# Kernel tuning notes

Measured on AMD Instinct MI355X. Metric: run time of the kernel, lower is better.

Reference implementation:

```python
import jax, jax.numpy as jnp
import numpy as np

N, E1, E2, P, H = 4096, 131072, 131072, 65536, 128
ROLE_VOCAB, ROLE_DIM, IDX_VOCAB, IDX_DIM = 8, 16, 1024, 8


def _lin_init(key, fan_in, fan_out):
    k1, k2 = jax.random.split(key)
    bound = 1.0 / np.sqrt(fan_in)
    W = jax.random.uniform(k1, (fan_in, fan_out), jnp.float32, -bound, bound)
    b = jax.random.uniform(k2, (fan_out,), jnp.float32, -bound, bound)
    return W, b


def setup_inputs() -> dict:
    key = jax.random.key(0)
    ks = jax.random.split(key, 24)
    d = {}
    d["block_features"] = jax.random.normal(ks[0], (N, 16), jnp.float32)
    d["role_ids"] = jax.random.randint(ks[1], (N,), 0, ROLE_VOCAB)
    d["b2b_src"] = jax.random.randint(ks[2], (E1,), 0, N)
    d["b2b_dst"] = jax.random.randint(ks[3], (E1,), 0, N)
    d["b2b_w"] = jax.random.uniform(ks[4], (E1,), jnp.float32)
    d["p2b_pin"] = jax.random.randint(ks[5], (E2,), 0, P)
    d["p2b_block"] = jax.random.randint(ks[6], (E2,), 0, N)
    d["p2b_w"] = jax.random.uniform(ks[7], (E2,), jnp.float32)
    d["pins_pos"] = jax.random.normal(ks[8], (P, 2), jnp.float32)
    d["area_targets"] = jax.random.uniform(ks[9], (N,), jnp.float32)
    # parameters
    d["role_emb"] = jax.random.normal(ks[10], (ROLE_VOCAB, ROLE_DIM), jnp.float32)
    d["idx_emb"] = jax.random.normal(ks[11], (IDX_VOCAB, IDX_DIM), jnp.float32)
    d["in_W1"], d["in_b1"] = _lin_init(ks[12], 16 + IDX_DIM + ROLE_DIM, H)
    d["in_W2"], d["in_b2"] = _lin_init(ks[13], H, H)
    d["b2b_W1"], d["b2b_b1"] = _lin_init(ks[14], 2 * H + 1, H)
    d["b2b_W2"], d["b2b_b2"] = _lin_init(ks[15], H, H)
    d["p2b_W1"], d["p2b_b1"] = _lin_init(ks[16], H + 3, H)
    d["p2b_W2"], d["p2b_b2"] = _lin_init(ks[17], H, H)
    d["self_W"], d["self_b"] = _lin_init(ks[18], H, H)
    d["ln_g"] = jnp.ones((H,), jnp.float32)
    d["ln_b"] = jnp.zeros((H,), jnp.float32)
    d["gp_W1"], d["gp_b1"] = _lin_init(ks[19], 2 * H, H)
    d["gp_W2"], d["gp_b2"] = _lin_init(ks[20], H, H)
    return d


def _mlp2(x, W1, b1, W2, b2):
    return jax.nn.relu(x @ W1 + b1) @ W2 + b2


def _forward(block_features, role_ids, b2b_src, b2b_dst, b2b_w, p2b_pin, p2b_block,
             p2b_w, pins_pos, area_targets, role_emb, idx_emb, in_W1, in_b1, in_W2,
             in_b2, b2b_W1, b2b_b1, b2b_W2, b2b_b2, p2b_W1, p2b_b1, p2b_W2, p2b_b2,
             self_W, self_b, ln_g, ln_b, gp_W1, gp_b1, gp_W2, gp_b2):
    n = block_features.shape[0]
    role_e = role_emb[role_ids]                       # [N, role_dim]
    idx_e = idx_emb[jnp.arange(n) % IDX_VOCAB]        # [N, idx_dim]
    x = jnp.concatenate([block_features, role_e, idx_e], axis=-1)
    h = jax.nn.relu(_mlp2(x, in_W1, in_b1, in_W2, in_b2))  # input_proj ends in ReLU

    # --- b2b messages: two directed messages per undirected edge ---
    max_b2b = jax.lax.stop_gradient(jnp.maximum(jnp.max(jnp.abs(b2b_w)), 1.0))
    w = (b2b_w / max_b2b)[:, None]                    # [E1, 1]
    hi, hj = h[b2b_src], h[b2b_dst]                   # [E1, H]
    m_ij = _mlp2(jnp.concatenate([hi, hj, w], -1), b2b_W1, b2b_b1, b2b_W2, b2b_b2)
    m_ji = _mlp2(jnp.concatenate([hj, hi, w], -1), b2b_W1, b2b_b1, b2b_W2, b2b_b2)
    agg = jnp.zeros_like(h).at[b2b_src].add(m_ij).at[b2b_dst].add(m_ji)

    # --- p2b messages ---
    total_area = jnp.maximum(jnp.sum(area_targets), 1e-6)
    case_scale = jax.lax.stop_gradient(jnp.maximum(jnp.sqrt(total_area), 1e-6))
    max_p2b = jax.lax.stop_gradient(jnp.maximum(jnp.max(jnp.abs(p2b_w)), 1.0))
    pin_feats = jnp.concatenate(
        [pins_pos[p2b_pin] / case_scale, (p2b_w / max_p2b)[:, None]], axis=-1)  # [E2, 3]
    m_p = _mlp2(jnp.concatenate([h[p2b_block], pin_feats], -1),
                p2b_W1, p2b_b1, p2b_W2, p2b_b2)
    agg = agg.at[p2b_block].add(m_p)

    # --- combine + LayerNorm ---
    z = h @ self_W + self_b + agg
    mu = jnp.mean(z, axis=-1, keepdims=True)
    var = jnp.mean(jnp.square(z - mu), axis=-1, keepdims=True)
    block_embeddings = (z - mu) / jnp.sqrt(var + 1e-5) * ln_g + ln_b

    pooled = jnp.concatenate(
        [block_embeddings.mean(axis=0), block_embeddings.max(axis=0)], axis=-1)
    graph_embedding = _mlp2(pooled, gp_W1, gp_b1, gp_W2, gp_b2)
    return block_embeddings, graph_embedding


def reference(block_features, role_ids, b2b_src, b2b_dst, b2b_w, p2b_pin, p2b_block,
              p2b_w, pins_pos, area_targets, role_emb, idx_emb, in_W1, in_b1, in_W2,
              in_b2, b2b_W1, b2b_b1, b2b_W2, b2b_b2, p2b_W1, p2b_b1, p2b_W2, p2b_b2,
              self_W, self_b, ln_g, ln_b, gp_W1, gp_b1, gp_W2, gp_b2):
    block_embeddings, graph_embedding = _forward(
        block_features, role_ids, b2b_src, b2b_dst, b2b_w, p2b_pin, p2b_block,
        p2b_w, pins_pos, area_targets, role_emb, idx_emb, in_W1, in_b1, in_W2,
        in_b2, b2b_W1, b2b_b1, b2b_W2, b2b_b2, p2b_W1, p2b_b1, p2b_W2, p2b_b2,
        self_W, self_b, ln_g, ln_b, gp_W1, gp_b1, gp_W2, gp_b2)
    block_mask = jnp.ones((block_features.shape[0],), dtype=bool)
    return block_embeddings, graph_embedding, block_mask
```

## Files before the change

kernel.cpp:

```cpp
#include <hip/hip_runtime.h>
#include <hip/hip_bf16.h>

#define N_NODES 4096
#define HDIM    128
#define E1      131072
#define E2      131072
#define NMSG_B2B (2 * E1)
#define CAPB    192
#define CAPP    96
#define STGB    128
#define STGP    64

#define OFF_CNTB   8
#define OFF_CNTP   (OFF_CNTB + 4096)
#define OFF_RED    (OFF_CNTP + 4096)
#define OFF_PSUM   (OFF_RED + 96)
#define OFF_PMAX   (OFF_PSUM + 128)
#define OFF_HB     (OFF_PMAX + 128)
#define OFF_P      (OFF_HB + 262144)
#define OFF_Q      (OFF_P + 524288)
#define OFF_R      (OFF_Q + 524288)
#define OFF_CP     (OFF_R + 524288)
#define OFF_B2H    (OFF_CP + 24576)
#define OFF_B2L    (OFF_B2H + 8192)
#define OFF_P2H    (OFF_B2L + 8192)
#define OFF_P2L    (OFF_P2H + 8192)
#define OFF_SWP    (OFF_P2L + 8192)
#define OFF_IW1    (OFF_SWP + 8192)
#define OFF_IW2    (OFF_IW1 + 4096)
#define OFF_WLAST  (OFF_IW2 + 8192)
#define OFF_PEXTRA (OFF_WLAST + 128)
#define OFF_BKB    (OFF_PEXTRA + 384)
#define OFF_BKP    (OFF_BKB + 2 * N_NODES * CAPB)
#define WS_FLOATS  (OFF_BKP + 2 * N_NODES * CAPP)

typedef short short8 __attribute__((ext_vector_type(8)));
typedef float f32x4 __attribute__((ext_vector_type(4)));

__device__ __forceinline__ unsigned short f2bf(float f) {
  union { float f; unsigned u; } v; v.f = f;
  unsigned r = v.u + 0x7fffu + ((v.u >> 16) & 1u);
  return (unsigned short)(r >> 16);
}
__device__ __forceinline__ float bf2f(unsigned short h) {
  return __uint_as_float((unsigned)h << 16);
}
__device__ __forceinline__ int il(int c) { return ((c & 63) << 1) | (c >> 6); }
__device__ __forceinline__ f32x4 relu4(f32x4 v) {
  f32x4 r;
  r[0] = fmaxf(v[0], 0.f); r[1] = fmaxf(v[1], 0.f);
  r[2] = fmaxf(v[2], 0.f); r[3] = fmaxf(v[3], 0.f);
  return r;
}

__global__ __launch_bounds__(256) void setup_kernel(const float* __restrict__ b2bw,
                                                    const float* __restrict__ p2bw,
                                                    const float* __restrict__ area,
                                                    const float* __restrict__ bW1,
                                                    const float* __restrict__ bW2,
                                                    const float* __restrict__ pW1,
                                                    const float* __restrict__ pW2,
                                                    const float* __restrict__ sWm,
                                                    const float* __restrict__ iW1,
                                                    const float* __restrict__ iW2,
                                                    const int* __restrict__ src,
                                                    const int* __restrict__ dst,
                                                    const int* __restrict__ pblk,
                                                    const int* __restrict__ ppin,
                                                    const float* __restrict__ pins,
                                                    float* __restrict__ ws) {
  __shared__ float red[256];
  int b = blockIdx.x, t = threadIdx.x;
  if (b < 32) {
    float m = 0.f;
    for (int i = b * 256 + t; i < E1; i += 32 * 256) m = fmaxf(m, fabsf(b2bw[i]));
    red[t] = m; __syncthreads();
    for (int s = 128; s > 0; s >>= 1) { if (t < s) red[t] = fmaxf(red[t], red[t + s]); __syncthreads(); }
    if (t == 0) ws[OFF_RED + b] = red[0];
  } else if (b < 64) {
    float m = 0.f;
    for (int i = (b - 32) * 256 + t; i < E2; i += 32 * 256) m = fmaxf(m, fabsf(p2bw[i]));
    red[t] = m; __syncthreads();
    for (int s = 128; s > 0; s >>= 1) { if (t < s) red[t] = fmaxf(red[t], red[t + s]); __syncthreads(); }
    if (t == 0) ws[OFF_RED + b] = red[0];
  } else if (b < 96) {
    float s0 = 0.f;
    for (int i = (b - 64) * 256 + t; i < N_NODES; i += 32 * 256) s0 += area[i];
    red[t] = s0; __syncthreads();
    for (int s = 128; s > 0; s >>= 1) { if (t < s) red[t] += red[t + s]; __syncthreads(); }
    if (t == 0) ws[OFF_RED + b] = red[0];
  } else if (b == 96) {
    if (t < HDIM) {
      ws[OFF_PSUM + t] = 0.f;
      ((int*)ws)[OFF_PMAX + t] = 0x80000000;
    }
  } else if (b < 225) {
    unsigned short* Cp  = (unsigned short*)(ws + OFF_CP);
    unsigned short* B2h = (unsigned short*)(ws + OFF_B2H);
    unsigned short* B2l = (unsigned short*)(ws + OFF_B2L);
    unsigned short* P2h = (unsigned short*)(ws + OFF_P2H);
    unsigned short* P2l = (unsigned short*)(ws + OFF_P2L);
    unsigned short* Swp = (unsigned short*)(ws + OFF_SWP);
    unsigned short* I1p = (unsigned short*)(ws + OFF_IW1);
    unsigned short* I2p = (unsigned short*)(ws + OFF_IW2);
    float* wlast = ws + OFF_WLAST;
    float* pextra = ws + OFF_PEXTRA;
    const int total = 156160;
    for (int x = (b - 97) * 256 + t; x < total; x += 128 * 256) {
      if (x < 49152) {
        int j = x & 7, lane = (x >> 3) & 63, ks = (x >> 9) & 3, nc = x >> 11;
        int col = nc * 16 + (lane & 15), k = ks * 32 + (lane >> 4) * 8 + j;
        float v;
        if (col < 128)      v = bW1[k * 128 + col];
        else if (col < 256) v = bW1[(128 + k) * 128 + (col - 128)];
        else                v = pW1[k * 128 + (col - 256)];
        Cp[x] = f2bf(v);
      } else if (x < 114688) {
        int u = (x - 49152) & 16383, which = (x - 49152) >> 14;
        int j = u & 7, lane = (u >> 3) & 63, ks = (u >> 9) & 3, nt = u >> 11;
        int n = nt * 16 + (lane & 15), k = ks * 32 + (lane >> 4) * 8 + j;
        float v = (which < 2) ? bW2[k * 128 + n] : pW2[k * 128 + n];
        unsigned short hi = f2bf(v);
        unsigned short outv = (which & 1) ? f2bf(v - bf2f(hi)) : hi;
        ((which < 2) ? ((which & 1) ? B2l : B2h) : ((which & 1) ? P2l : P2h))[u] = outv;
      } else if (x < 131072) {
        int u = x - 114688;
        int j = u & 7, lane = (u >> 3) & 63, ks = (u >> 9) & 3, nt = u >> 11;
        int n = nt * 16 + (lane & 15), k = ks * 32 + (lane >> 4) * 8 + j;
        Swp[u] = f2bf(sWm[k * 128 + n]);
      } else if (x < 139264) {
        int u = x - 131072;
        int j = u & 7, lane = (u >> 3) & 63, ks = (u >> 9) & 1, nt = u >> 10;
        int n = nt * 16 + (lane & 15), k = ks * 32 + (lane >> 4) * 8 + j;
        I1p[u] = (k < 40) ? f2bf(iW1[k * 128 + n]) : 0;
      } else if (x < 155648) {
        int u = x - 139264;
        int j = u & 7, lane = (u >> 3) & 63, ks = (u >> 9) & 3, nt = u >> 11;
        int n = nt * 16 + (lane & 15), k = ks * 32 + (lane >> 4) * 8 + j;
        I2p[u] = f2bf(iW2[k * 128 + n]);
      } else if (x < 155776) {
        int c = x - 155648;
        wlast[il(c)] = bW1[256 * 128 + c];
      } else {
        int u = x - 155776;
        int r = u >> 7, c = u & 127;
        pextra[r * 128 + il(c)] = pW1[(128 + r) * 128 + c];
      }
    }
  } else {
    int i = (b - 225) * 256 + t;
    int* cntB = (int*)ws + OFF_CNTB;
    int* cntP = (int*)ws + OFF_CNTP;
    uint2* BKB = (uint2*)((int*)ws + OFF_BKB);
    uint2* BKP = (uint2*)((int*)ws + OFF_BKP);
    if (i < NMSG_B2B) {
      int e = i >> 1, d = i & 1;
      int tg = d ? dst[e] : src[e];
      int o  = d ? src[e] : dst[e];
      int pos = atomicAdd(&cntB[tg], 1);
      if (pos < CAPB) {
        uint2 v; v.x = (unsigned)o; v.y = __float_as_uint(b2bw[e]);
        BKB[tg * CAPB + pos] = v;
      }
    } else {
      int e = i - NMSG_B2B;
      int pin = ppin[e];
      int tg = pblk[e];
      int pos = atomicAdd(&cntP[tg], 1);
      if (pos < CAPP) {
        uint2 v;
        v.x = ((unsigned)f2bf(pins[pin * 2 + 1]) << 16) | (unsigned)f2bf(pins[pin * 2]);
        v.y = __float_as_uint(p2bw[e]);
        BKP[tg * CAPP + pos] = v;
      }
    }
  }
}

__global__ __launch_bounds__(512) void mid_kernel(const float* __restrict__ bfeat,
                                                  const int* __restrict__ rid,
                                                  const float* __restrict__ remb,
                                                  const float* __restrict__ iemb,
                                                  const float* __restrict__ ib1,
                                                  const float* __restrict__ ib2,
                                                  const float* __restrict__ bb1,
                                                  const float* __restrict__ pb1,
                                                  float* __restrict__ ws,
                                                  unsigned short* __restrict__ hb) {
  __shared__ __attribute__((aligned(16))) unsigned short xs[16 * 72];
  __shared__ __attribute__((aligned(16))) unsigned short h1s[16 * 136];
  __shared__ __attribute__((aligned(16))) unsigned short hs[16 * 136];
  int tid = threadIdx.x;
  const unsigned short* I1p = (const unsigned short*)(ws + OFF_IW1);
  const unsigned short* I2p = (const unsigned short*)(ws + OFF_IW2);
  const unsigned short* Cp  = (const unsigned short*)(ws + OFF_CP);
  float* P = ws + OFF_P;
  float* Q = ws + OFF_Q;
  float* R = ws + OFF_R;
  int n0 = blockIdx.x * 16;
  for (int idx = tid; idx < 1024; idx += 512) {
    int m = idx >> 6, c = idx & 63;
    int n = n0 + m;
    float v = 0.f;
    if (c < 16)      v = bfeat[n * 16 + c];
    else if (c < 32) v = remb[rid[n] * 16 + (c - 16)];
    else if (c < 40) v = iemb[(n & 1023) * 8 + (c - 32)];
    xs[m * 72 + c] = f2bf(v);
  }
  __syncthreads();
  int lane = tid & 63, wv = tid >> 6;
  int l15 = lane & 15, q = lane >> 4;
  f32x4 zero = {0.f, 0.f, 0.f, 0.f};
  f32x4 a1 = zero;
#pragma unroll
  for (int ks = 0; ks < 2; ks++) {
    short8 af = *(const short8*)(&xs[l15 * 72 + ks * 32 + q * 8]);
    short8 bfr = *(const short8*)(I1p + ((wv * 2 + ks) * 64 + lane) * 8);
    a1 = __builtin_amdgcn_mfma_f32_16x16x32_bf16(af, bfr, a1, 0, 0, 0);
  }
  {
    int n = wv * 16 + l15;
    float b = ib1[n];
#pragma unroll
    for (int r = 0; r < 4; r++)
      h1s[(q * 4 + r) * 136 + n] = f2bf(fmaxf(a1[r] + b, 0.f));
  }
  __syncthreads();
  f32x4 a2 = zero;
#pragma unroll
  for (int ks = 0; ks < 4; ks++) {
    short8 af = *(const short8*)(&h1s[l15 * 136 + ks * 32 + q * 8]);
    short8 bfr = *(const short8*)(I2p + ((wv * 4 + ks) * 64 + lane) * 8);
    a2 = __builtin_amdgcn_mfma_f32_16x16x32_bf16(af, bfr, a2, 0, 0, 0);
  }
  {
    int n = wv * 16 + l15;
    float b = ib2[n];
#pragma unroll
    for (int r = 0; r < 4; r++) {
      unsigned short hv = f2bf(fmaxf(a2[r] + b, 0.f));
      hs[(q * 4 + r) * 136 + n] = hv;
      hb[(n0 + q * 4 + r) * 128 + n] = hv;
    }
  }
  __syncthreads();
  f32x4 a3[3];
#pragma unroll
  for (int i = 0; i < 3; i++) a3[i] = zero;
#pragma unroll
  for (int ks = 0; ks < 4; ks++) {
    short8 af = *(const short8*)(&hs[l15 * 136 + ks * 32 + q * 8]);
#pragma unroll
    for (int j = 0; j < 3; j++) {
      short8 bfr = *(const short8*)(Cp + (((3 * wv + j) * 4 + ks) * 64 + lane) * 8);
      a3[j] = __builtin_amdgcn_mfma_f32_16x16x32_bf16(af, bfr, a3[j], 0, 0, 0);
    }
  }
#pragma unroll
  for (int j = 0; j < 3; j++) {
    int col = (3 * wv + j) * 16 + l15;
    int arr = col >> 7, cc = col & 127;
    float bias = (arr == 0) ? bb1[cc] : ((arr == 2) ? pb1[cc] : 0.f);
    float* dstp = (arr == 0) ? P : ((arr == 1) ? Q : R);
    int ic = il(cc);
#pragma unroll
    for (int r = 0; r < 4; r++)
      dstp[(n0 + q * 4 + r) * 128 + ic] = a3[j][r] + bias;
  }
}

__global__ __launch_bounds__(1024) void fused_kernel(const unsigned short* __restrict__ hb,
                                                     const float* __restrict__ sb,
                                                     const float* __restrict__ lng,
                                                     const float* __restrict__ lnb,
                                                     const float* __restrict__ bb2,
                                                     const float* __restrict__ pb2,
                                                     const float* __restrict__ gW1,
                                                     const float* __restrict__ gb1,
                                                     const float* __restrict__ gW2,
                                                     const float* __restrict__ gb2,
                                                     float* __restrict__ ws,
                                                     float* __restrict__ out) {
  __shared__ __attribute__((aligned(16))) unsigned short A[16 * 648];
  __shared__ __attribute__((aligned(16))) union {
    struct { float zp[2][16 * 128]; float zs[16 * 133]; } t;
    struct { uint2 bkb[16][STGB]; uint2 bkp[16][STGP]; } e;
  } U;
  __shared__ float muS[16], rsg[16];
  __shared__ float partS[16][16], partQ[16][16];
  __shared__ float psumL[8][128];
  __shared__ int   pmaxL[8][128];
  __shared__ float sInvB, sInvP, sInvC;
  __shared__ int   isLast;
  int tid = threadIdx.x;
  int n0 = blockIdx.x * 16;
  int lane = tid & 63, wv = tid >> 6;
  const int* cntBp = (const int*)ws + OFF_CNTB;
  const int* cntPp = (const int*)ws + OFF_CNTP;
  const uint2* BKB = (const uint2*)((const int*)ws + OFF_BKB);
  const uint2* BKP = (const uint2*)((const int*)ws + OFF_BKP);
  if (tid < 256) {
    int m = tid >> 4, o = (tid & 15) * 8;
    *(uint4*)(&A[m * 648 + o]) = *(const uint4*)(hb + (n0 + m) * 128 + o);
  }
  for (int idx = tid; idx < 16 * STGB; idx += 1024) {
    int m = idx >> 7, j = idx & (STGB - 1);
    if (j < cntBp[n0 + m]) U.e.bkb[m][j] = BKB[(n0 + m) * CAPB + j];
  }
  {
    int m = tid >> 6, j = tid & (STGP - 1);
    if (tid < 16 * STGP && j < cntPp[n0 + m]) U.e.bkp[m][j] = BKP[(n0 + m) * CAPP + j];
  }
  if (tid < 96) {
    float v = ws[OFF_RED + tid];
    if (tid < 64) {
#pragma unroll
      for (int s = 1; s < 32; s <<= 1) v = fmaxf(v, __shfl_xor(v, s, 64));
      if (tid == 0)  sInvB = 1.f / fmaxf(v, 1.f);
      if (tid == 32) sInvP = 1.f / fmaxf(v, 1.f);
    } else {
#pragma unroll
      for (int s = 1; s < 32; s <<= 1) v += __shfl_xor(v, s, 64);
      if (tid == 64) {
        float cs = fmaxf(sqrtf(fmaxf(v, 1e-6f)), 1e-6f);
        sInvC = 1.f / cs;
      }
    }
  }
  int l5 = lane & 31, hf = lane >> 5;
  f32x4 wl = *(const f32x4*)(ws + OFF_WLAST + 4 * l5);
  f32x4 e0 = *(const f32x4*)(ws + OFF_PEXTRA + 4 * l5);
  f32x4 e1 = *(const f32x4*)(ws + OFF_PEXTRA + 128 + 4 * l5);
  f32x4 e2 = *(const f32x4*)(ws + OFF_PEXTRA + 256 + 4 * l5);
  __syncthreads();
  {
    const float* Pm = ws + OFF_P;
    const float* Qm = ws + OFF_Q;
    const float* Rm = ws + OFF_R;
    float invb = sInvB, invp = sInvP, invc = sInvC;
    wl *= invb; e0 *= invc; e1 *= invc; e2 *= invp;
    int ln = wv;
    int node = n0 + ln;
    {
      int cnt = min(cntBp[node], CAPB);
      int stg = min(cnt, STGB);
      const uint2* bkL = U.e.bkb[ln];
      const uint2* bkG = BKB + node * CAPB;
      f32x4 p4 = *(const f32x4*)(Pm + node * 128 + 4 * l5);
      f32x4 acc = {0.f, 0.f, 0.f, 0.f};
      int m = 0;
      for (; m + 16 <= stg; m += 16) {
        uint2 k0 = bkL[m + hf],      k1 = bkL[m + 2 + hf];
        uint2 k2 = bkL[m + 4 + hf],  k3 = bkL[m + 6 + hf];
        uint2 k4 = bkL[m + 8 + hf],  k5 = bkL[m + 10 + hf];
        uint2 k6 = bkL[m + 12 + hf], k7 = bkL[m + 14 + hf];
        f32x4 q0 = *(const f32x4*)(Qm + k0.x * 128 + 4 * l5);
        f32x4 q1 = *(const f32x4*)(Qm + k1.x * 128 + 4 * l5);
        f32x4 q2 = *(const f32x4*)(Qm + k2.x * 128 + 4 * l5);
        f32x4 q3 = *(const f32x4*)(Qm + k3.x * 128 + 4 * l5);
        f32x4 q4 = *(const f32x4*)(Qm + k4.x * 128 + 4 * l5);
        f32x4 q5 = *(const f32x4*)(Qm + k5.x * 128 + 4 * l5);
        f32x4 q6 = *(const f32x4*)(Qm + k6.x * 128 + 4 * l5);
        f32x4 q7 = *(const f32x4*)(Qm + k7.x * 128 + 4 * l5);
        acc += relu4(p4 + __uint_as_float(k0.y) * wl + q0);
        acc += relu4(p4 + __uint_as_float(k1.y) * wl + q1);
        acc += relu4(p4 + __uint_as_float(k2.y) * wl + q2);
        acc += relu4(p4 + __uint_as_float(k3.y) * wl + q3);
        acc += relu4(p4 + __uint_as_float(k4.y) * wl + q4);
        acc += relu4(p4 + __uint_as_float(k5.y) * wl + q5);
        acc += relu4(p4 + __uint_as_float(k6.y) * wl + q6);
        acc += relu4(p4 + __uint_as_float(k7.y) * wl + q7);
      }
      for (; m + 8 <= stg; m += 8) {
        uint2 k0 = bkL[m + hf],     k1 = bkL[m + 2 + hf];
        uint2 k2 = bkL[m + 4 + hf], k3 = bkL[m + 6 + hf];
        f32x4 q0 = *(const f32x4*)(Qm + k0.x * 128 + 4 * l5);
        f32x4 q1 = *(const f32x4*)(Qm + k1.x * 128 + 4 * l5);
        f32x4 q2 = *(const f32x4*)(Qm + k2.x * 128 + 4 * l5);
        f32x4 q3 = *(const f32x4*)(Qm + k3.x * 128 + 4 * l5);
        acc += relu4(p4 + __uint_as_float(k0.y) * wl + q0);
        acc += relu4(p4 + __uint_as_float(k1.y) * wl + q1);
        acc += relu4(p4 + __uint_as_float(k2.y) * wl + q2);
        acc += relu4(p4 + __uint_as_float(k3.y) * wl + q3);
      }
      for (; m + 2 <= stg; m += 2) {
        uint2 k = bkL[m + hf];
        f32x4 q = *(const f32x4*)(Qm + k.x * 128 + 4 * l5);
        acc += relu4(p4 + __uint_as_float(k.y) * wl + q);
      }
      if (m < stg) {
        uint2 k = bkL[m + hf];
        f32x4 q = *(const f32x4*)(Qm + (k.x & (N_NODES - 1)) * 128 + 4 * l5);
        f32x4 v = relu4(p4 + __uint_as_float(k.y) * wl + q);
        if (hf == 0) acc += v;
        m++;
      }
      for (; m + 2 <= cnt; m += 2) {
        uint2 k = bkG[m + hf];
        f32x4 q = *(const f32x4*)(Qm + k.x * 128 + 4 * l5);
        acc += relu4(p4 + __uint_as_float(k.y) * wl + q);
      }
      if (m < cnt) {
        uint2 k = bkG[m + hf];
        f32x4 q = *(const f32x4*)(Qm + (k.x & (N_NODES - 1)) * 128 + 4 * l5);
        f32x4 v = relu4(p4 + __uint_as_float(k.y) * wl + q);
        if (hf == 0) acc += v;
      }
      f32x4 tot;
#pragma unroll
      for (int j = 0; j < 4; j++) tot[j] = acc[j] + __shfl_xor(acc[j], 32, 64);
      if (hf == 0) {
        unsigned short h0 = f2bf(tot[0]), h1 = f2bf(tot[1]);
        unsigned short h2 = f2bf(tot[2]), h3 = f2bf(tot[3]);
        *(unsigned*)(&A[ln * 648 + 128 + 2 * l5])      = (unsigned)h0 | ((unsigned)h2 << 16);
        *(unsigned*)(&A[ln * 648 + 128 + 64 + 2 * l5]) = (unsigned)h1 | ((unsigned)h3 << 16);
        unsigned short g0 = f2bf(tot[0] - bf2f(h0)), g1 = f2bf(tot[1] - bf2f(h1));
        unsigned short g2 = f2bf(tot[2] - bf2f(h2)), g3 = f2bf(tot[3] - bf2f(h3));
        *(unsigned*)(&A[ln * 648 + 256 + 2 * l5])      = (unsigned)g0 | ((unsigned)g2 << 16);
        *(unsigned*)(&A[ln * 648 + 256 + 64 + 2 * l5]) = (unsigned)g1 | ((unsigned)g3 << 16);
      }
    }
    {
      int cnt = min(cntPp[node], CAPP);
      int stg = min(cnt, STGP);
      const uint2* bkL = U.e.bkp[ln];
      const uint2* bkG = BKP + node * CAPP;
      f32x4 r4 = *(const f32x4*)(Rm + node * 128 + 4 * l5);
      f32x4 acc = {0.f, 0.f, 0.f, 0.f};
      int m = 0;
      for (; m + 4 <= stg; m += 4) {
        uint2 ka = bkL[m + hf], kb = bkL[m + 2 + hf];
        float a0 = __uint_as_float((ka.x & 0xFFFFu) << 16);
        float a1 = __uint_as_float(ka.x & 0xFFFF0000u);
        float a2 = __uint_as_float(ka.y);
        float b0 = __uint_as_float((kb.x & 0xFFFFu) << 16);
        float b1 = __uint_as_float(kb.x & 0xFFFF0000u);
        float b2 = __uint_as_float(kb.y);
        acc += relu4(r4 + a0 * e0 + a1 * e1 + a2 * e2);
        acc += relu4(r4 + b0 * e0 + b1 * e1 + b2 * e2);
      }
      for (; m + 2 <= stg; m += 2) {
        uint2 ka = bkL[m + hf];
        float a0 = __uint_as_float((ka.x & 0xFFFFu) << 16);
        float a1 = __uint_as_float(ka.x & 0xFFFF0000u);
        float a2 = __uint_as_float(ka.y);
        acc += relu4(r4 + a0 * e0 + a1 * e1 + a2 * e2);
      }
      if (m < stg) {
        uint2 ka = bkL[m + hf];
        float a0 = __uint_as_float((ka.x & 0xFFFFu) << 16);
        float a1 = __uint_as_float(ka.x & 0xFFFF0000u);
        float a2 = __uint_as_float(ka.y);
        f32x4 v = relu4(r4 + a0 * e0 + a1 * e1 + a2 * e2);
        if (hf == 0) acc += v;
        m++;
      }
      for (; m + 2 <= cnt; m += 2) {
        uint2 ka = bkG[m + hf];
        float a0 = __uint_as_float((ka.x & 0xFFFFu) << 16);
        float a1 = __uint_as_float(ka.x & 0xFFFF0000u);
        float a2 = __uint_as_float(ka.y);
        acc += relu4(r4 + a0 * e0 + a1 * e1 + a2 * e2);
      }
      if (m < cnt) {
        uint2 ka = bkG[m + hf];
        float a0 = __uint_as_float((ka.x & 0xFFFFu) << 16);
        float a1 = __uint_as_float(ka.x & 0xFFFF0000u);
        float a2 = __uint_as_float(ka.y);
        f32x4 v = relu4(r4 + a0 * e0 + a1 * e1 + a2 * e2);
        if (hf == 0) acc += v;
      }
      f32x4 tot;
#pragma unroll
      for (int j = 0; j < 4; j++) tot[j] = acc[j] + __shfl_xor(acc[j], 32, 64);
      if (hf == 0) {
        unsigned short h0 = f2bf(tot[0]), h1 = f2bf(tot[1]);
        unsigned short h2 = f2bf(tot[2]), h3 = f2bf(tot[3]);
        *(unsigned*)(&A[ln * 648 + 384 + 2 * l5])      = (unsigned)h0 | ((unsigned)h2 << 16);
        *(unsigned*)(&A[ln * 648 + 384 + 64 + 2 * l5]) = (unsigned)h1 | ((unsigned)h3 << 16);
        unsigned short g0 = f2bf(tot[0] - bf2f(h0)), g1 = f2bf(tot[1] - bf2f(h1));
        unsigned short g2 = f2bf(tot[2] - bf2f(h2)), g3 = f2bf(tot[3] - bf2f(h3));
        *(unsigned*)(&A[ln * 648 + 512 + 2 * l5])      = (unsigned)g0 | ((unsigned)g2 << 16);
        *(unsigned*)(&A[ln * 648 + 512 + 64 + 2 * l5]) = (unsigned)g1 | ((unsigned)g3 << 16);
      }
    }
  }
  __syncthreads();
  int l15 = lane & 15, q = lane >> 4;
  int ct = wv & 7, half = wv >> 3;
  f32x4 zero = {0.f, 0.f, 0.f, 0.f};
  f32x4 acc = zero;
  const unsigned short* bufs[7] = {
    (const unsigned short*)(ws + OFF_SWP), (const unsigned short*)(ws + OFF_B2H),
    (const unsigned short*)(ws + OFF_B2L), (const unsigned short*)(ws + OFF_B2H),
    (const unsigned short*)(ws + OFF_P2H), (const unsigned short*)(ws + OFF_P2L),
    (const unsigned short*)(ws + OFF_P2H)};
  const int segs[7] = {0, 128, 128, 256, 384, 384, 512};
  int p0 = half ? 4 : 0, p1 = half ? 7 : 4;
  for (int p = p0; p < p1; p++) {
#pragma unroll
    for (int ks = 0; ks < 4; ks++) {
      short8 af = *(const short8*)(&A[l15 * 648 + segs[p] + ks * 32 + q * 8]);
      short8 bfr = *(const short8*)(bufs[p] + ((ct * 4 + ks) * 64 + lane) * 8);
      acc = __builtin_amdgcn_mfma_f32_16x16x32_bf16(af, bfr, acc, 0, 0, 0);
    }
  }
  {
    int nn = ct * 16 + l15;
#pragma unroll
    for (int r = 0; r < 4; r++)
      U.t.zp[half][(q * 4 + r) * 128 + nn] = acc[r];
  }
  __syncthreads();
  {
    int idx = tid;
    for (int rep = 0; rep < 2; rep++, idx += 1024) {
      int row = idx >> 7, c = idx & 127;
      float cb = (float)cntBp[n0 + row], cp = (float)cntPp[n0 + row];
      U.t.zs[row * 133 + c] = U.t.zp[0][row * 128 + c] + U.t.zp[1][row * 128 + c]
                            + sb[c] + cb * bb2[c] + cp * pb2[c];
    }
  }
  __syncthreads();
  if (tid < 256) {
    int r = tid >> 4, g = tid & 15;
    const float* zr = &U.t.zs[r * 133 + g * 8];
    float s = 0.f, s2 = 0.f;
#pragma unroll
    for (int i = 0; i < 8; i++) { float v = zr[i]; s += v; s2 += v * v; }
    partS[r][g] = s; partQ[r][g] = s2;
  }
  __syncthreads();
  if (tid < 16) {
    float s = 0.f, s2 = 0.f;
#pragma unroll
    for (int g = 0; g < 16; g++) { s += partS[tid][g]; s2 += partQ[tid][g]; }
    float m = s * (1.f / 128.f);
    float var = s2 * (1.f / 128.f) - m * m;
    muS[tid] = m;
    rsg[tid] = rsqrtf(fmaxf(var, 0.f) + 1e-5f);
  }
  __syncthreads();
  {
    int c = tid & 127, grp = tid >> 7;
    float g = lng[c], b = lnb[c];
    float ls = 0.f; int lm = 0x80000000;
    for (int r = grp * 2; r < grp * 2 + 2; r++) {
      float v = (U.t.zs[r * 133 + c] - muS[r]) * rsg[r] * g + b;
      out[(n0 + r) * 128 + c] = v;
      ls += v;
      int e = __float_as_int(v);
      e = e >= 0 ? e : (e ^ 0x7fffffff);
      lm = max(lm, e);
    }
    psumL[grp][c] = ls; pmaxL[grp][c] = lm;
  }
  __syncthreads();
  if (tid < 128) {
    float s = 0.f; int mx = 0x80000000;
#pragma unroll
    for (int g = 0; g < 8; g++) { s += psumL[g][tid]; mx = max(mx, pmaxL[g][tid]); }
    atomicAdd(&ws[OFF_PSUM + tid], s);
    atomicMax(&((int*)ws)[OFF_PMAX + tid], mx);
  }
  if (tid < 16) out[N_NODES * HDIM + HDIM + n0 + tid] = 1.0f;
  __syncthreads();
  if (tid == 0) {
    __threadfence();
    int v = atomicAdd(&((int*)ws)[3], 1);
    isLast = (v == (int)gridDim.x - 1);
  }
  __syncthreads();
  if (!isLast) return;
  __shared__ float pooled[256];
  __shared__ float gpart[8][128];
  __shared__ float g1[128];
  if (tid < 128) {
    pooled[tid] = atomicAdd(&ws[OFF_PSUM + tid], 0.f) * (1.f / (float)N_NODES);
  } else if (tid < 256) {
    int e = atomicAdd(&((int*)ws)[OFF_PMAX + (tid - 128)], 0);
    int bits = e >= 0 ? e : (e ^ 0x7fffffff);
    pooled[tid] = __int_as_float(bits);
  }
  __syncthreads();
  {
    int c = tid & 127, g = tid >> 7;
    float acc2 = 0.f;
#pragma unroll 8
    for (int k = g * 32; k < g * 32 + 32; k++) acc2 += pooled[k] * gW1[k * 128 + c];
    gpart[g][c] = acc2;
  }
  __syncthreads();
  if (tid < 128) {
    float s = gb1[tid];
#pragma unroll
    for (int g = 0; g < 8; g++) s += gpart[g][tid];
    g1[tid] = fmaxf(s, 0.f);
  }
  __syncthreads();
  {
    int c = tid & 127, g = tid >> 7;
    float acc2 = 0.f;
#pragma unroll 8
    for (int k = g * 16; k < g * 16 + 16; k++) acc2 += g1[k] * gW2[k * 128 + c];
    gpart[g][c] = acc2;
  }
  __syncthreads();
  if (tid < 128) {
    float s = gb2[tid];
#pragma unroll
    for (int g = 0; g < 8; g++) s += gpart[g][tid];
    out[N_NODES * HDIM + tid] = s;
  }
}

extern "C" void kernel_launch(void* const* d_in, const int* in_sizes, int n_in,
                              void* d_out, int out_size, void* d_ws, size_t ws_size,
                              hipStream_t stream) {
  const float* bfeat = (const float*)d_in[0];
  const int*   rid   = (const int*)d_in[1];
  const int*   bsrc  = (const int*)d_in[2];
  const int*   bdst  = (const int*)d_in[3];
  const float* bw    = (const float*)d_in[4];
  const int*   ppin  = (const int*)d_in[5];
  const int*   pblk  = (const int*)d_in[6];
  const float* pw    = (const float*)d_in[7];
  const float* pins  = (const float*)d_in[8];
  const float* area  = (const float*)d_in[9];
  const float* remb  = (const float*)d_in[10];
  const float* iemb  = (const float*)d_in[11];
  const float* inW1  = (const float*)d_in[12];
  const float* inb1  = (const float*)d_in[13];
  const float* inW2  = (const float*)d_in[14];
  const float* inb2  = (const float*)d_in[15];
  const float* bW1   = (const float*)d_in[16];
  const float* bb1   = (const float*)d_in[17];
  const float* bW2   = (const float*)d_in[18];
  const float* bb2   = (const float*)d_in[19];
  const float* pW1   = (const float*)d_in[20];
  const float* pb1   = (const float*)d_in[21];
  const float* pW2   = (const float*)d_in[22];
  const float* pb2   = (const float*)d_in[23];
  const float* sW    = (const float*)d_in[24];
  const float* sb    = (const float*)d_in[25];
  const float* lng   = (const float*)d_in[26];
  const float* lnb   = (const float*)d_in[27];
  const float* gW1   = (const float*)d_in[28];
  const float* gb1   = (const float*)d_in[29];
  const float* gW2   = (const float*)d_in[30];
  const float* gb2   = (const float*)d_in[31];

  float* ws  = (float*)d_ws;
  float* out = (float*)d_out;
  unsigned short* hb = (unsigned short*)(ws + OFF_HB);

  hipMemsetAsync(d_ws, 0, OFF_RED * sizeof(float), stream);
  setup_kernel<<<1761, 256, 0, stream>>>(bw, pw, area,
                                         bW1, bW2, pW1, pW2, sW, inW1, inW2,
                                         bsrc, bdst, pblk, ppin, pins, ws);
  mid_kernel<<<256, 512, 0, stream>>>(bfeat, rid, remb, iemb, inb1, inb2, bb1, pb1,
                                      ws, hb);
  fused_kernel<<<256, 1024, 0, stream>>>(hb, sb, lng, lnb, bb2, pb2,
                                         gW1, gb1, gW2, gb2, ws, out);
}
```

Baseline: 189.2 us.

## Merge setup and input-MLP kernels, converting weights to bf16 on the fly

Folds the former mid_kernel (input MLP and P/Q/R projection) into the setup kernel as extra blocks, so one launch does reductions, weight packing, edge bucketing and the node MLP. The input-MLP and first-layer edge weights are no longer pre-packed into bf16 MFMA layout in workspace. Each block instead reads them as fp32 from global memory and rounds them per lane. This removes one kernel launch and the dependency between packing and use. The cost is strided, uncoalesced fp32 weight reads repeated by all 256 MLP blocks, and the blocks now run alongside the bucketing atomics.

```diff
diff --git a/kernel.cpp b/kernel.cpp
--- a/kernel.cpp
+++ b/kernel.cpp
@@ -53,102 +53,98 @@
   return r;
 }
 
-__global__ __launch_bounds__(256) void setup_kernel(const float* __restrict__ b2bw,
-                                                    const float* __restrict__ p2bw,
-                                                    const float* __restrict__ area,
-                                                    const float* __restrict__ bW1,
-                                                    const float* __restrict__ bW2,
-                                                    const float* __restrict__ pW1,
-                                                    const float* __restrict__ pW2,
-                                                    const float* __restrict__ sWm,
-                                                    const float* __restrict__ iW1,
-                                                    const float* __restrict__ iW2,
-                                                    const int* __restrict__ src,
-                                                    const int* __restrict__ dst,
-                                                    const int* __restrict__ pblk,
-                                                    const int* __restrict__ ppin,
-                                                    const float* __restrict__ pins,
-                                                    float* __restrict__ ws) {
-  __shared__ float red[256];
+__global__ __launch_bounds__(512) void prep_kernel(const float* __restrict__ b2bw,
+                                                   const float* __restrict__ p2bw,
+                                                   const float* __restrict__ area,
+                                                   const float* __restrict__ bW1,
+                                                   const float* __restrict__ bW2,
+                                                   const float* __restrict__ pW1,
+                                                   const float* __restrict__ pW2,
+                                                   const float* __restrict__ sWm,
+                                                   const float* __restrict__ iW1,
+                                                   const float* __restrict__ iW2,
+                                                   const int* __restrict__ src,
+                                                   const int* __restrict__ dst,
+                                                   const int* __restrict__ pblk,
+                                                   const int* __restrict__ ppin,
+                                                   const float* __restrict__ pins,
+                                                   const float* __restrict__ bfeat,
+                                                   const int* __restrict__ rid,
+                                                   const float* __restrict__ remb,
+                                                   const float* __restrict__ iemb,
+                                                   const float* __restrict__ ib1,
+                                                   const float* __restrict__ ib2,
+                                                   const float* __restrict__ bb1,
+                                                   const float* __restrict__ pb1,
+                                                   float* __restrict__ ws,
+                                                   unsigned short* __restrict__ hb) {
   int b = blockIdx.x, t = threadIdx.x;
-  if (b < 32) {
-    float m = 0.f;
-    for (int i = b * 256 + t; i < E1; i += 32 * 256) m = fmaxf(m, fabsf(b2bw[i]));
-    red[t] = m; __syncthreads();
-    for (int s = 128; s > 0; s >>= 1) { if (t < s) red[t] = fmaxf(red[t], red[t + s]); __syncthreads(); }
-    if (t == 0) ws[OFF_RED + b] = red[0];
-  } else if (b < 64) {
-    float m = 0.f;
-    for (int i = (b - 32) * 256 + t; i < E2; i += 32 * 256) m = fmaxf(m, fabsf(p2bw[i]));
-    red[t] = m; __syncthreads();
-    for (int s = 128; s > 0; s >>= 1) { if (t < s) red[t] = fmaxf(red[t], red[t + s]); __syncthreads(); }
-    if (t == 0) ws[OFF_RED + b] = red[0];
-  } else if (b < 96) {
-    float s0 = 0.f;
-    for (int i = (b - 64) * 256 + t; i < N_NODES; i += 32 * 256) s0 += area[i];
-    red[t] = s0; __syncthreads();
-    for (int s = 128; s > 0; s >>= 1) { if (t < s) red[t] += red[t + s]; __syncthreads(); }
-    if (t == 0) ws[OFF_RED + b] = red[0];
-  } else if (b == 96) {
+  if (b < 96) {
+    __shared__ float red[512];
+    if (b < 32) {
+      float m = 0.f;
+      for (int i = b * 512 + t; i < E1; i += 32 * 512) m = fmaxf(m, fabsf(b2bw[i]));
+      red[t] = m; __syncthreads();
+      for (int s = 256; s > 0; s >>= 1) { if (t < s) red[t] = fmaxf(red[t], red[t + s]); __syncthreads(); }
+      if (t == 0) ws[OFF_RED + b] = red[0];
+    } else if (b < 64) {
+      float m = 0.f;
+      for (int i = (b - 32) * 512 + t; i < E2; i += 32 * 512) m = fmaxf(m, fabsf(p2bw[i]));
+      red[t] = m; __syncthreads();
+      for (int s = 256; s > 0; s >>= 1) { if (t < s) red[t] = fmaxf(red[t], red[t + s]); __syncthreads(); }
+      if (t == 0) ws[OFF_RED + b] = red[0];
+    } else {
+      float s0 = 0.f;
+      for (int i = (b - 64) * 512 + t; i < N_NODES; i += 32 * 512) s0 += area[i];
+      red[t] = s0; __syncthreads();
+      for (int s = 256; s > 0; s >>= 1) { if (t < s) red[t] += red[t + s]; __syncthreads(); }
+      if (t == 0) ws[OFF_RED + b] = red[0];
+    }
+    return;
+  }
+  if (b == 96) {
     if (t < HDIM) {
       ws[OFF_PSUM + t] = 0.f;
       ((int*)ws)[OFF_PMAX + t] = 0x80000000;
     }
-  } else if (b < 225) {
-    unsigned short* Cp  = (unsigned short*)(ws + OFF_CP);
+    return;
+  }
+  if (b < 161) {
     unsigned short* B2h = (unsigned short*)(ws + OFF_B2H);
     unsigned short* B2l = (unsigned short*)(ws + OFF_B2L);
     unsigned short* P2h = (unsigned short*)(ws + OFF_P2H);
     unsigned short* P2l = (unsigned short*)(ws + OFF_P2L);
     unsigned short* Swp = (unsigned short*)(ws + OFF_SWP);
-    unsigned short* I1p = (unsigned short*)(ws + OFF_IW1);
-    unsigned short* I2p = (unsigned short*)(ws + OFF_IW2);
     float* wlast = ws + OFF_WLAST;
     float* pextra = ws + OFF_PEXTRA;
-    const int total = 156160;
-    for (int x = (b - 97) * 256 + t; x < total; x += 128 * 256) {
-      if (x < 49152) {
-        int j = x & 7, lane = (x >> 3) & 63, ks = (x >> 9) & 3, nc = x >> 11;
-        int col = nc * 16 + (lane & 15), k = ks * 32 + (lane >> 4) * 8 + j;
-        float v;
-        if (col < 128)      v = bW1[k * 128 + col];
-        else if (col < 256) v = bW1[(128 + k) * 128 + (col - 128)];
-        else                v = pW1[k * 128 + (col - 256)];
-        Cp[x] = f2bf(v);
-      } else if (x < 114688) {
-        int u = (x - 49152) & 16383, which = (x - 49152) >> 14;
+    const int total = 82432;
+    for (int x = (b - 97) * 512 + t; x < total; x += 64 * 512) {
+      if (x < 65536) {
+        int u = x & 16383, which = x >> 14;
         int j = u & 7, lane = (u >> 3) & 63, ks = (u >> 9) & 3, nt = u >> 11;
         int n = nt * 16 + (lane & 15), k = ks * 32 + (lane >> 4) * 8 + j;
         float v = (which < 2) ? bW2[k * 128 + n] : pW2[k * 128 + n];
         unsigned short hi = f2bf(v);
         unsigned short outv = (which & 1) ? f2bf(v - bf2f(hi)) : hi;
         ((which < 2) ? ((which & 1) ? B2l : B2h) : ((which & 1) ? P2l : P2h))[u] = outv;
-      } else if (x < 131072) {
-        int u = x - 114688;
+      } else if (x < 81920) {
+        int u = x - 65536;
         int j = u & 7, lane = (u >> 3) & 63, ks = (u >> 9) & 3, nt = u >> 11;
         int n = nt * 16 + (lane & 15), k = ks * 32 + (lane >> 4) * 8 + j;
         Swp[u] = f2bf(sWm[k * 128 + n]);
-      } else if (x < 139264) {
-        int u = x - 131072;
-        int j = u & 7, lane = (u >> 3) & 63, ks = (u >> 9) & 1, nt = u >> 10;
-        int n = nt * 16 + (lane & 15), k = ks * 32 + (lane >> 4) * 8 + j;
-        I1p[u] = (k < 40) ? f2bf(iW1[k * 128 + n]) : 0;
-      } else if (x < 155648) {
-        int u = x - 139264;
-        int j = u & 7, lane = (u >> 3) & 63, ks = (u >> 9) & 3, nt = u >> 11;
-        int n = nt * 16 + (lane & 15), k = ks * 32 + (lane >> 4) * 8 + j;
-        I2p[u] = f2bf(iW2[k * 128 + n]);
-      } else if (x < 155776) {
-        int c = x - 155648;
+      } else if (x < 82048) {
+        int c = x - 81920;
         wlast[il(c)] = bW1[256 * 128 + c];
       } else {
-        int u = x - 155776;
+        int u = x - 82048;
         int r = u >> 7, c = u & 127;
         pextra[r * 128 + il(c)] = pW1[(128 + r) * 128 + c];
       }
     }
-  } else {
-    int i = (b - 225) * 256 + t;
+    return;
+  }
+  if (b < 929) {
+    int i = (b - 161) * 512 + t;
     int* cntB = (int*)ws + OFF_CNTB;
     int* cntP = (int*)ws + OFF_CNTP;
     uint2* BKB = (uint2*)((int*)ws + OFF_BKB);
@@ -174,31 +170,16 @@
         BKP[tg * CAPP + pos] = v;
       }
     }
-  }
-}
-
-__global__ __launch_bounds__(512) void mid_kernel(const float* __restrict__ bfeat,
-                                                  const int* __restrict__ rid,
-                                                  const float* __restrict__ remb,
-                                                  const float* __restrict__ iemb,
-                                                  const float* __restrict__ ib1,
-                                                  const float* __restrict__ ib2,
-                                                  const float* __restrict__ bb1,
-                                                  const float* __restrict__ pb1,
-                                                  float* __restrict__ ws,
-                                                  unsigned short* __restrict__ hb) {
+    return;
+  }
   __shared__ __attribute__((aligned(16))) unsigned short xs[16 * 72];
   __shared__ __attribute__((aligned(16))) unsigned short h1s[16 * 136];
   __shared__ __attribute__((aligned(16))) unsigned short hs[16 * 136];
-  int tid = threadIdx.x;
-  const unsigned short* I1p = (const unsigned short*)(ws + OFF_IW1);
-  const unsigned short* I2p = (const unsigned short*)(ws + OFF_IW2);
-  const unsigned short* Cp  = (const unsigned short*)(ws + OFF_CP);
   float* P = ws + OFF_P;
   float* Q = ws + OFF_Q;
   float* R = ws + OFF_R;
-  int n0 = blockIdx.x * 16;
-  for (int idx = tid; idx < 1024; idx += 512) {
+  int n0 = (b - 929) * 16;
+  for (int idx = t; idx < 1024; idx += 512) {
     int m = idx >> 6, c = idx & 63;
     int n = n0 + m;
     float v = 0.f;
@@ -208,39 +189,48 @@
     xs[m * 72 + c] = f2bf(v);
   }
   __syncthreads();
-  int lane = tid & 63, wv = tid >> 6;
+  int lane = t & 63, wv = t >> 6;
   int l15 = lane & 15, q = lane >> 4;
+  int nW = wv * 16 + l15;
   f32x4 zero = {0.f, 0.f, 0.f, 0.f};
   f32x4 a1 = zero;
 #pragma unroll
   for (int ks = 0; ks < 2; ks++) {
     short8 af = *(const short8*)(&xs[l15 * 72 + ks * 32 + q * 8]);
-    short8 bfr = *(const short8*)(I1p + ((wv * 2 + ks) * 64 + lane) * 8);
+    short8 bfr;
+#pragma unroll
+    for (int j = 0; j < 8; j++) {
+      int k = ks * 32 + q * 8 + j;
+      bfr[j] = (short)((k < 40) ? f2bf(iW1[k * 128 + nW]) : (unsigned short)0);
+    }
     a1 = __builtin_amdgcn_mfma_f32_16x16x32_bf16(af, bfr, a1, 0, 0, 0);
   }
   {
-    int n = wv * 16 + l15;
-    float b = ib1[n];
+    float bv = ib1[nW];
 #pragma unroll
     for (int r = 0; r < 4; r++)
-      h1s[(q * 4 + r) * 136 + n] = f2bf(fmaxf(a1[r] + b, 0.f));
+      h1s[(q * 4 + r) * 136 + nW] = f2bf(fmaxf(a1[r] + bv, 0.f));
   }
   __syncthreads();
   f32x4 a2 = zero;
 #pragma unroll
   for (int ks = 0; ks < 4; ks++) {
     short8 af = *(const short8*)(&h1s[l15 * 136 + ks * 32 + q * 8]);
-    short8 bfr = *(const short8*)(I2p + ((wv * 4 + ks) * 64 + lane) * 8);
+    short8 bfr;
+#pragma unroll
+    for (int j = 0; j < 8; j++) {
+      int k = ks * 32 + q * 8 + j;
+      bfr[j] = (short)f2bf(iW2[k * 128 + nW]);
+    }
     a2 = __builtin_amdgcn_mfma_f32_16x16x32_bf16(af, bfr, a2, 0, 0, 0);
   }
   {
-    int n = wv * 16 + l15;
-    float b = ib2[n];
+    float bv = ib2[nW];
 #pragma unroll
     for (int r = 0; r < 4; r++) {
-      unsigned short hv = f2bf(fmaxf(a2[r] + b, 0.f));
-      hs[(q * 4 + r) * 136 + n] = hv;
-      hb[(n0 + q * 4 + r) * 128 + n] = hv;
+      unsigned short hv = f2bf(fmaxf(a2[r] + bv, 0.f));
+      hs[(q * 4 + r) * 136 + nW] = hv;
+      hb[(n0 + q * 4 + r) * 128 + nW] = hv;
     }
   }
   __syncthreads();
@@ -252,7 +242,18 @@
     short8 af = *(const short8*)(&hs[l15 * 136 + ks * 32 + q * 8]);
 #pragma unroll
     for (int j = 0; j < 3; j++) {
-      short8 bfr = *(const short8*)(Cp + (((3 * wv + j) * 4 + ks) * 64 + lane) * 8);
+      int col = (3 * wv + j) * 16 + l15;
+      const float* srcW;
+      int c2;
+      if (col < 128)      { srcW = bW1;             c2 = col; }
+      else if (col < 256) { srcW = bW1 + 128 * 128; c2 = col - 128; }
+      else                { srcW = pW1;             c2 = col - 256; }
+      short8 bfr;
+#pragma unroll
+      for (int jj = 0; jj < 8; jj++) {
+        int k = ks * 32 + q * 8 + jj;
+        bfr[jj] = (short)f2bf(srcW[k * 128 + c2]);
+      }
       a3[j] = __builtin_amdgcn_mfma_f32_16x16x32_bf16(af, bfr, a3[j], 0, 0, 0);
     }
   }
@@ -655,11 +656,11 @@
   unsigned short* hb = (unsigned short*)(ws + OFF_HB);
 
   hipMemsetAsync(d_ws, 0, OFF_RED * sizeof(float), stream);
-  setup_kernel<<<1761, 256, 0, stream>>>(bw, pw, area,
-                                         bW1, bW2, pW1, pW2, sW, inW1, inW2,
-                                         bsrc, bdst, pblk, ppin, pins, ws);
-  mid_kernel<<<256, 512, 0, stream>>>(bfeat, rid, remb, iemb, inb1, inb2, bb1, pb1,
-                                      ws, hb);
+  prep_kernel<<<1185, 512, 0, stream>>>(bw, pw, area,
+                                        bW1, bW2, pW1, pW2, sW, inW1, inW2,
+                                        bsrc, bdst, pblk, ppin, pins,
+                                        bfeat, rid, remb, iemb, inb1, inb2, bb1, pb1,
+                                        ws, hb);
   fused_kernel<<<256, 1024, 0, stream>>>(hb, sb, lng, lnb, bb2, pb2,
                                          gW1, gb1, gW2, gb2, ws, out);
 }
```

Result: slower. 194.2 us (+2.6%).
